# Kernel tuning notes

Measured on AMD Instinct MI355X. Metric: run time of the kernel, lower is better.

## Reference

```python
import jax, jax.numpy as jnp
import numpy as np
import math

NEG_INF = -1e9  # large negative used as masked-logit value (pre-scaling, as in the original)


def setup_inputs() -> dict:
    key = jax.random.key(0)
    k1, k2, k3 = jax.random.split(key, 3)
    bs, ql, kl, d = 8, 2048, 2048, 512
    return {
        "query": jax.random.normal(k1, (bs, ql, d), dtype=jnp.float32),
        "key": jax.random.normal(k2, (bs, kl, d), dtype=jnp.float32),
        "value": jax.random.normal(k3, (bs, kl, d), dtype=jnp.float32),
        "use_mask": 1,
        "cell_dim": 512,
    }


def reference(query, key, value, use_mask, cell_dim):
    bs, ql, d = query.shape[0], query.shape[1], value.shape[2]
    kl = key.shape[1]
    # [bs, ql, kl] raw scores
    mm = jnp.einsum("bqd,bkd->bqk", query, key)
    if use_mask:
        # mask positions where key index > query index (strictly future)
        q_idx = jnp.arange(ql)[:, None]
        k_idx = jnp.arange(kl)[None, :]
        mask = (k_idx > q_idx).astype(mm.dtype)  # [ql, kl]
        mm = mm + mask[None, :, :] * NEG_INF
    # log_softmax(...).exp() == softmax, computed stably in one pass
    w = jax.nn.softmax(mm / math.sqrt(cell_dim), axis=2)
    # weighted value aggregation (original broadcasts to [bs,ql,kl,d]; einsum fuses it)
    res = jnp.einsum("bqk,bkd->bqd", w, value)
    return res
```

## Files before the change

kernel.cpp:

```cpp
#include <hip/hip_runtime.h>
#include <math.h>

typedef __bf16 bf16x8 __attribute__((ext_vector_type(8)));
typedef float floatx4 __attribute__((ext_vector_type(4)));
typedef unsigned short ushort8_t __attribute__((ext_vector_type(8)));

#define BSZ 8
#define SEQ 2048
#define DIM 512
#define BKEY 32
#define BQ 128
#define NSLOT 70

__device__ __forceinline__ unsigned short f2bf(float f) {
    unsigned int u = __float_as_uint(f);
    u += 0x7fffu + ((u >> 16) & 1u);
    return (unsigned short)(u >> 16);
}
__device__ __forceinline__ float bf2f(unsigned short s) {
    return __uint_as_float(((unsigned int)s) << 16);
}

#define ASYNC16(g, l) __builtin_amdgcn_global_load_lds( \
    (const __attribute__((address_space(1))) unsigned int*)(g), \
    (__attribute__((address_space(3))) unsigned int*)(l), 16, 0, 0)

__global__ __launch_bounds__(256) void conv_k(const float* __restrict__ K,
                                              unsigned short* __restrict__ Kb) {
    size_t i = ((size_t)blockIdx.x * 256 + threadIdx.x) * 8;
    float4 a = *(const float4*)(K + i);
    float4 b = *(const float4*)(K + i + 4);
    ushort8_t u;
    u[0]=f2bf(a.x); u[1]=f2bf(a.y); u[2]=f2bf(a.z); u[3]=f2bf(a.w);
    u[4]=f2bf(b.x); u[5]=f2bf(b.y); u[6]=f2bf(b.z); u[7]=f2bf(b.w);
    *(ushort8_t*)(Kb + i) = u;
}

__global__ __launch_bounds__(256) void trans_v(const float* __restrict__ V,
                                               unsigned short* __restrict__ Vt) {
    __shared__ unsigned short T[BKEY][DIM + 8];
    const int bid = blockIdx.x;
    const int b = bid & 7, kb = bid >> 3;
    const float* src = V + ((size_t)b * SEQ + (size_t)kb * BKEY) * DIM;
    const int tid = threadIdx.x;
    #pragma unroll
    for (int i = 0; i < 16; ++i) {
        const int idx = i * 256 + tid;
        const int key = idx >> 7;
        const int d = (idx & 127) * 4;
        float4 x = *(const float4*)(src + (size_t)key * DIM + d);
        T[key][d]   = f2bf(x.x);
        T[key][d+1] = f2bf(x.y);
        T[key][d+2] = f2bf(x.z);
        T[key][d+3] = f2bf(x.w);
    }
    __syncthreads();
    unsigned short* dst = Vt + (size_t)(b * (SEQ / BKEY) + kb) * DIM * BKEY;
    #pragma unroll
    for (int i = 0; i < 8; ++i) {
        const int cidx = i * 256 + tid;
        const int d = cidx >> 2;
        const int kc = cidx & 3;
        ushort8_t v;
        #pragma unroll
        for (int k2 = 0; k2 < 8; ++k2) v[k2] = T[kc * 8 + k2][d];
        *(ushort8_t*)(dst + cidx * 8) = v;
    }
}


template <int SPLIT>
__global__ __launch_bounds__(512, 2)
void attn_fwd(const float* __restrict__ Q,
              const unsigned short* __restrict__ Kb,
              const unsigned short* __restrict__ Vt,
              unsigned short* __restrict__ PartO,
              float* __restrict__ Pml,
              float* __restrict__ O)
{
    __shared__ unsigned short Ksh[2][BKEY * DIM];
    __shared__ unsigned short Vsh[2][DIM * BKEY];
    __shared__ unsigned short Psh[8 * 16 * BKEY];

    const int tid  = threadIdx.x;
    const int lane = tid & 63;
    const int wv   = tid >> 6;
    const int ml   = lane & 15;
    const int quad = lane >> 4;

    const int bid = blockIdx.x;
    const int b   = bid & 7;
    const int j   = bid >> 3;
    int t, c;
    if (SPLIT) {
        t = 15; c = j;
        while (true) { const int cnt = (t + 2) >> 1; if (c < cnt) break; c -= cnt; --t; }
    } else { t = 15 - j; c = 0; }
    const int kt0 = c * 8;
    const int nk  = 4 * t + 4;
    const int kt1 = min(kt0 + 8, nk);
    const bool is_split = SPLIT && (t >= 2);
    const int q0 = t * BQ;
    const int kdiag = 4 * t;

    const float* Qb = Q + (size_t)b * SEQ * DIM;
    const unsigned short* Kbb = Kb + (size_t)b * SEQ * DIM;
    const unsigned short* Vtb = Vt + (size_t)b * SEQ * DIM;
    float* Ob = O + (size_t)b * SEQ * DIM;

    bf16x8 qf[16];
    {
        const float* qp = Qb + (size_t)(q0 + wv * 16 + ml) * DIM + quad * 8;
        #pragma unroll
        for (int kc = 0; kc < 16; ++kc) {
            float4 x = *(const float4*)(qp + kc * 32);
            float4 y = *(const float4*)(qp + kc * 32 + 4);
            union { bf16x8 v; unsigned short s[8]; } u;
            u.s[0]=f2bf(x.x); u.s[1]=f2bf(x.y); u.s[2]=f2bf(x.z); u.s[3]=f2bf(x.w);
            u.s[4]=f2bf(y.x); u.s[5]=f2bf(y.y); u.s[6]=f2bf(y.z); u.s[7]=f2bf(y.w);
            qf[kc] = u.v;
        }
    }
    asm volatile("" ::: "memory");

    floatx4 acc[32];
    #pragma unroll
    for (int i = 0; i < 32; ++i) acc[i] = (floatx4){0.f, 0.f, 0.f, 0.f};
    float mrun[4] = {-INFINITY, -INFINITY, -INFINITY, -INFINITY};
    float lrun[4] = {0.f, 0.f, 0.f, 0.f};

    const float CS = 1.4426950408889634f * 0.04419417382415922f;

    #define STAGE_K(buf_, kt_) do { \
        const unsigned short* Kt_ = Kbb + (size_t)(kt_) * (BKEY * DIM); \
        unsigned short* Kd_ = &Ksh[(buf_)][0]; \
        _Pragma("unroll") \
        for (int i_ = 0; i_ < 4; ++i_) { \
            const int ci_  = i_ * 512 + tid; \
            const int row_ = ci_ >> 6; \
            const int ch_  = (ci_ & 63) ^ (row_ & 7); \
            ASYNC16(Kt_ + (size_t)row_ * DIM + ch_ * 8, Kd_ + ci_ * 8); \
        } } while (0)
    #define STAGE_V(buf_, kt_) do { \
        const unsigned short* Vt_ = Vtb + (size_t)(kt_) * (DIM * BKEY); \
        unsigned short* Vd_ = &Vsh[(buf_)][0]; \
        _Pragma("unroll") \
        for (int i_ = 0; i_ < 4; ++i_) { \
            const int ci_ = i_ * 512 + tid; \
            const int d_  = ci_ >> 2; \
            const int kc_ = (ci_ & 3) ^ (d_ & 3); \
            ASYNC16(Vt_ + d_ * BKEY + kc_ * 8, Vd_ + ci_ * 8); \
        } } while (0)

    STAGE_K(0, kt0);
    STAGE_V(0, kt0);
    asm volatile("s_waitcnt vmcnt(4)" ::: "memory");
    __builtin_amdgcn_s_barrier();

    int cur = 0;
    for (int kt = kt0; kt < kt1; ++kt) {
        const int k0 = kt * BKEY;
        const bool havenxt = (kt + 1 < kt1);

        if (havenxt) STAGE_K(cur ^ 1, kt + 1);

        const unsigned short* Ks = &Ksh[cur][0];
        floatx4 s0 = (floatx4){0,0,0,0}, s1 = (floatx4){0,0,0,0};
        floatx4 s0b = (floatx4){0,0,0,0}, s1b = (floatx4){0,0,0,0};
        const int sw = ml & 7;
        __builtin_amdgcn_s_setprio(1);
        #pragma unroll
        for (int kc = 0; kc < 16; kc += 2) {
            const int ch0 = kc * 4 + quad, ch1 = (kc + 1) * 4 + quad;
            bf16x8 a0 = *(bf16x8*)&Ks[ml * DIM + ((ch0 ^ sw) << 3)];
            bf16x8 a1 = *(bf16x8*)&Ks[(16 + ml) * DIM + ((ch0 ^ sw) << 3)];
            bf16x8 b0 = *(bf16x8*)&Ks[ml * DIM + ((ch1 ^ sw) << 3)];
            bf16x8 b1 = *(bf16x8*)&Ks[(16 + ml) * DIM + ((ch1 ^ sw) << 3)];
            s0  = __builtin_amdgcn_mfma_f32_16x16x32_bf16(qf[kc],     a0, s0,  0, 0, 0);
            s1  = __builtin_amdgcn_mfma_f32_16x16x32_bf16(qf[kc],     a1, s1,  0, 0, 0);
            s0b = __builtin_amdgcn_mfma_f32_16x16x32_bf16(qf[kc + 1], b0, s0b, 0, 0, 0);
            s1b = __builtin_amdgcn_mfma_f32_16x16x32_bf16(qf[kc + 1], b1, s1b, 0, 0, 0);
        }
        __builtin_amdgcn_s_setprio(0);
        s0 = s0 + s0b;
        s1 = s1 + s1b;

        float z[2][4], pr[2][4], al[4], rs[4];
        if (kt >= kdiag) {
            #pragma unroll
            for (int r = 0; r < 4; ++r) {
                const int qg = q0 + wv * 16 + quad * 4 + r;
                z[0][r] = (k0 + ml > qg)      ? -INFINITY : s0[r] * CS;
                z[1][r] = (k0 + 16 + ml > qg) ? -INFINITY : s1[r] * CS;
            }
        } else {
            #pragma unroll
            for (int r = 0; r < 4; ++r) { z[0][r] = s0[r] * CS; z[1][r] = s1[r] * CS; }
        }
        #pragma unroll
        for (int r = 0; r < 4; ++r) {
            float v = fmaxf(z[0][r], z[1][r]);
            v = fmaxf(v, __shfl_xor(v, 1, 64));
            v = fmaxf(v, __shfl_xor(v, 2, 64));
            v = fmaxf(v, __shfl_xor(v, 4, 64));
            v = fmaxf(v, __shfl_xor(v, 8, 64));
            const float nm = fmaxf(mrun[r], v);
            al[r]   = __builtin_amdgcn_exp2f(mrun[r] - nm);
            mrun[r] = nm;
        }
        #pragma unroll
        for (int r = 0; r < 4; ++r) {
            pr[0][r] = __builtin_amdgcn_exp2f(z[0][r] - mrun[r]);
            pr[1][r] = __builtin_amdgcn_exp2f(z[1][r] - mrun[r]);
            float s = pr[0][r] + pr[1][r];
            s += __shfl_xor(s, 1, 64);
            s += __shfl_xor(s, 2, 64);
            s += __shfl_xor(s, 4, 64);
            s += __shfl_xor(s, 8, 64);
            rs[r] = s;
        }
        #pragma unroll
        for (int r = 0; r < 4; ++r) lrun[r] = lrun[r] * al[r] + rs[r];

        if (al[0] < 1.f || al[1] < 1.f || al[2] < 1.f || al[3] < 1.f) {
            #pragma unroll
            for (int nt = 0; nt < 32; ++nt) {
                acc[nt][0] *= al[0]; acc[nt][1] *= al[1];
                acc[nt][2] *= al[2]; acc[nt][3] *= al[3];
            }
        }

        unsigned short* Pw = &Psh[wv * (16 * BKEY)];
        #pragma unroll
        for (int nt = 0; nt < 2; ++nt) {
            #pragma unroll
            for (int r = 0; r < 4; ++r) {
                const int row = quad * 4 + r, col = nt * 16 + ml;
                Pw[row * BKEY + ((((col >> 3) ^ (row & 3)) << 3) | (col & 7))] = f2bf(pr[nt][r]);
            }
        }
        asm volatile("s_waitcnt lgkmcnt(0)" ::: "memory");
        bf16x8 pf = *(bf16x8*)&Pw[ml * BKEY + ((quad ^ (ml & 3)) << 3)];

        if (havenxt) { asm volatile("s_waitcnt vmcnt(4)" ::: "memory"); }
        else         { asm volatile("s_waitcnt vmcnt(0)" ::: "memory"); }
        __builtin_amdgcn_s_barrier();

        if (havenxt) STAGE_V(cur ^ 1, kt + 1);

        const unsigned short* Vs = &Vsh[cur][0];
        __builtin_amdgcn_s_setprio(1);
        #pragma unroll
        for (int nt = 0; nt < 32; ++nt) {
            const int drow = nt * 16 + ml;
            bf16x8 vf = *(bf16x8*)&Vs[drow * BKEY + ((quad ^ (drow & 3)) << 3)];
            acc[nt] = __builtin_amdgcn_mfma_f32_16x16x32_bf16(pf, vf, acc[nt], 0, 0, 0);
        }
        __builtin_amdgcn_s_setprio(0);

        if (havenxt) {
            asm volatile("s_waitcnt vmcnt(4)" ::: "memory");
            __builtin_amdgcn_s_barrier();
            cur ^= 1;
        }
    }
    #undef STAGE_K
    #undef STAGE_V

    if (!is_split) {
        float inv[4];
        #pragma unroll
        for (int r = 0; r < 4; ++r) inv[r] = 1.f / lrun[r];
        #pragma unroll
        for (int nt = 0; nt < 32; ++nt) {
            #pragma unroll
            for (int r = 0; r < 4; ++r) {
                const int row = q0 + wv * 16 + quad * 4 + r;
                Ob[(size_t)row * DIM + nt * 16 + ml] = acc[nt][r] * inv[r];
            }
        }
    } else {
        const size_t slot = (size_t)(b * NSLOT + j);
        unsigned short* po = PartO + slot * (BQ * DIM);
        #pragma unroll
        for (int nt = 0; nt < 32; ++nt) {
            #pragma unroll
            for (int r = 0; r < 4; ++r) {
                const int prow = wv * 16 + quad * 4 + r;
                po[prow * DIM + nt * 16 + ml] = f2bf(acc[nt][r]);
            }
        }
        if (ml == 0) {
            #pragma unroll
            for (int r = 0; r < 4; ++r) {
                const int prow = wv * 16 + quad * 4 + r;
                Pml[slot * 256 + prow * 2]     = mrun[r];
                Pml[slot * 256 + prow * 2 + 1] = lrun[r];
            }
        }
    }
}

__global__ __launch_bounds__(256)
void attn_merge(const unsigned short* __restrict__ PartO,
                const float* __restrict__ Pml,
                float* __restrict__ O)
{
    const int bid = blockIdx.x;
    const int b = bid & 7;
    const int u = bid >> 3;
    const int t = 2 + (u >> 2);
    const int rg = u & 3;
    const int nc = (t + 2) >> 1;
    int j0 = 0;
    for (int tp = 15; tp > t; --tp) j0 += (tp + 2) >> 1;

    const int r   = threadIdx.x >> 3;
    const int row = rg * 32 + r;
    const int d0  = (threadIdx.x & 7) * 64;

    float M = -INFINITY;
    for (int cc = 0; cc < nc; ++cc) {
        const size_t slot = (size_t)(b * NSLOT + j0 + cc);
        M = fmaxf(M, Pml[slot * 256 + row * 2]);
    }
    float L = 0.f;
    for (int cc = 0; cc < nc; ++cc) {
        const size_t slot = (size_t)(b * NSLOT + j0 + cc);
        L += Pml[slot * 256 + row * 2 + 1] *
             __builtin_amdgcn_exp2f(Pml[slot * 256 + row * 2] - M);
    }

    float o[64];
    #pragma unroll
    for (int i = 0; i < 64; ++i) o[i] = 0.f;
    for (int cc = 0; cc < nc; ++cc) {
        const size_t slot = (size_t)(b * NSLOT + j0 + cc);
        const float w = __builtin_amdgcn_exp2f(Pml[slot * 256 + row * 2] - M);
        const unsigned short* po = PartO + slot * (BQ * DIM) + (size_t)row * DIM + d0;
        #pragma unroll
        for (int i = 0; i < 8; ++i) {
            ushort8_t v = *(const ushort8_t*)(po + i * 8);
            #pragma unroll
            for (int k2 = 0; k2 < 8; ++k2) o[i * 8 + k2] += w * bf2f(v[k2]);
        }
    }
    const float invL = 1.f / L;
    float* out = O + ((size_t)b * SEQ + (size_t)t * BQ + row) * DIM + d0;
    #pragma unroll
    for (int i = 0; i < 16; ++i) {
        float4 v4 = { o[i*4] * invL, o[i*4+1] * invL, o[i*4+2] * invL, o[i*4+3] * invL };
        *(float4*)(out + i * 4) = v4;
    }
}

extern "C" void kernel_launch(void* const* d_in, const int* in_sizes, int n_in,
                              void* d_out, int out_size, void* d_ws, size_t ws_size,
                              hipStream_t stream) {
    const float* Q = (const float*)d_in[0];
    const float* K = (const float*)d_in[1];
    const float* V = (const float*)d_in[2];
    float* Out = (float*)d_out;

    const size_t elems = (size_t)BSZ * SEQ * DIM;
    unsigned short* Kb = (unsigned short*)d_ws;
    unsigned short* Vt = Kb + elems;
    unsigned short* PartO = Vt + elems;
    float* Pml = (float*)(PartO + (size_t)BSZ * NSLOT * BQ * DIM);

    const size_t need_split = 2 * elems * 2
                            + (size_t)BSZ * NSLOT * BQ * DIM * 2
                            + (size_t)BSZ * NSLOT * 256 * 4;
    conv_k<<<dim3(elems / 8 / 256), dim3(256), 0, stream>>>(K, Kb);
    trans_v<<<dim3(BSZ * (SEQ / BKEY)), dim3(256), 0, stream>>>(V, Vt);

    if (ws_size >= need_split) {
        attn_fwd<1><<<dim3(BSZ * 72), dim3(512), 0, stream>>>(Q, Kb, Vt, PartO, Pml, Out);
        attn_merge<<<dim3(BSZ * 14 * 4), dim3(256), 0, stream>>>(PartO, Pml, Out);
    } else {
        attn_fwd<0><<<dim3(BSZ * 16), dim3(512), 0, stream>>>(Q, Kb, Vt, PartO, Pml, Out);
    }
}
```

Before: 338.5 us.

## Shrink split-K chunks, fuse K/V prep kernels, and add lazy softmax rescaling

Parameterises the split-KV attention by chunk size and uses 6-key-tile chunks (96 blocks per batch) so work is spread more evenly across compute units, with a merge kernel that now covers more query tiles. The K conversion and V transpose kernels are merged into one launch to save a kernel launch. The online softmax now only raises the running max when the new max exceeds it by more than 8 in log2 units, which skips most accumulator rescales. The score registers are also reused in place for the probabilities. The lazy threshold allows exponentials up to 2^8 in bf16 P and fp32 sums, which is safe but changes rounding. Smaller chunks add partial-output traffic and merge work.

```diff
diff --git a/kernel.cpp b/kernel.cpp
--- a/kernel.cpp
+++ b/kernel.cpp
@@ -10,7 +10,6 @@
 #define DIM 512
 #define BKEY 32
 #define BQ 128
-#define NSLOT 70
 
 __device__ __forceinline__ unsigned short f2bf(float f) {
     unsigned int u = __float_as_uint(f);
@@ -25,21 +24,22 @@
     (const __attribute__((address_space(1))) unsigned int*)(g), \
     (__attribute__((address_space(3))) unsigned int*)(l), 16, 0, 0)
 
-__global__ __launch_bounds__(256) void conv_k(const float* __restrict__ K,
-                                              unsigned short* __restrict__ Kb) {
-    size_t i = ((size_t)blockIdx.x * 256 + threadIdx.x) * 8;
-    float4 a = *(const float4*)(K + i);
-    float4 b = *(const float4*)(K + i + 4);
-    ushort8_t u;
-    u[0]=f2bf(a.x); u[1]=f2bf(a.y); u[2]=f2bf(a.z); u[3]=f2bf(a.w);
-    u[4]=f2bf(b.x); u[5]=f2bf(b.y); u[6]=f2bf(b.z); u[7]=f2bf(b.w);
-    *(ushort8_t*)(Kb + i) = u;
-}
-
-__global__ __launch_bounds__(256) void trans_v(const float* __restrict__ V,
+__global__ __launch_bounds__(256) void prep_kv(const float* __restrict__ K,
+                                               const float* __restrict__ V,
+                                               unsigned short* __restrict__ Kb,
                                                unsigned short* __restrict__ Vt) {
+    if (blockIdx.x < 4096) {
+        size_t i = ((size_t)blockIdx.x * 256 + threadIdx.x) * 8;
+        float4 a = *(const float4*)(K + i);
+        float4 b = *(const float4*)(K + i + 4);
+        ushort8_t u;
+        u[0]=f2bf(a.x); u[1]=f2bf(a.y); u[2]=f2bf(a.z); u[3]=f2bf(a.w);
+        u[4]=f2bf(b.x); u[5]=f2bf(b.y); u[6]=f2bf(b.z); u[7]=f2bf(b.w);
+        *(ushort8_t*)(Kb + i) = u;
+        return;
+    }
     __shared__ unsigned short T[BKEY][DIM + 8];
-    const int bid = blockIdx.x;
+    const int bid = blockIdx.x - 4096;
     const int b = bid & 7, kb = bid >> 3;
     const float* src = V + ((size_t)b * SEQ + (size_t)kb * BKEY) * DIM;
     const int tid = threadIdx.x;
@@ -69,7 +69,7 @@
 }
 
 
-template <int SPLIT>
+template <int SPLIT, int CH, int NSLOT>
 __global__ __launch_bounds__(512, 2)
 void attn_fwd(const float* __restrict__ Q,
               const unsigned short* __restrict__ Kb,
@@ -94,12 +94,12 @@
     int t, c;
     if (SPLIT) {
         t = 15; c = j;
-        while (true) { const int cnt = (t + 2) >> 1; if (c < cnt) break; c -= cnt; --t; }
+        while (true) { const int cnt = (4 * t + 4 + CH - 1) / CH; if (c < cnt) break; c -= cnt; --t; }
     } else { t = 15 - j; c = 0; }
-    const int kt0 = c * 8;
     const int nk  = 4 * t + 4;
-    const int kt1 = min(kt0 + 8, nk);
-    const bool is_split = SPLIT && (t >= 2);
+    const int kt0 = c * CH;
+    const int kt1 = SPLIT ? min(kt0 + CH, nk) : nk;
+    const bool is_split = SPLIT && (nk > CH);
     const int q0 = t * BQ;
     const int kdiag = 4 * t;
 
@@ -126,7 +126,7 @@
     floatx4 acc[32];
     #pragma unroll
     for (int i = 0; i < 32; ++i) acc[i] = (floatx4){0.f, 0.f, 0.f, 0.f};
-    float mrun[4] = {-INFINITY, -INFINITY, -INFINITY, -INFINITY};
+    float mrun[4] = {-1e30f, -1e30f, -1e30f, -1e30f};
     float lrun[4] = {0.f, 0.f, 0.f, 0.f};
 
     const float CS = 1.4426950408889634f * 0.04419417382415922f;
@@ -185,42 +185,42 @@
         s0 = s0 + s0b;
         s1 = s1 + s1b;
 
-        float z[2][4], pr[2][4], al[4], rs[4];
         if (kt >= kdiag) {
             #pragma unroll
             for (int r = 0; r < 4; ++r) {
                 const int qg = q0 + wv * 16 + quad * 4 + r;
-                z[0][r] = (k0 + ml > qg)      ? -INFINITY : s0[r] * CS;
-                z[1][r] = (k0 + 16 + ml > qg) ? -INFINITY : s1[r] * CS;
+                s0[r] = (k0 + ml > qg)      ? -INFINITY : s0[r] * CS;
+                s1[r] = (k0 + 16 + ml > qg) ? -INFINITY : s1[r] * CS;
             }
         } else {
             #pragma unroll
-            for (int r = 0; r < 4; ++r) { z[0][r] = s0[r] * CS; z[1][r] = s1[r] * CS; }
-        }
+            for (int r = 0; r < 4; ++r) { s0[r] *= CS; s1[r] *= CS; }
+        }
+
+        float al[4];
         #pragma unroll
         for (int r = 0; r < 4; ++r) {
-            float v = fmaxf(z[0][r], z[1][r]);
+            float v = fmaxf(s0[r], s1[r]);
             v = fmaxf(v, __shfl_xor(v, 1, 64));
             v = fmaxf(v, __shfl_xor(v, 2, 64));
             v = fmaxf(v, __shfl_xor(v, 4, 64));
             v = fmaxf(v, __shfl_xor(v, 8, 64));
-            const float nm = fmaxf(mrun[r], v);
-            al[r]   = __builtin_amdgcn_exp2f(mrun[r] - nm);
-            mrun[r] = nm;
+            const float d = v - mrun[r];
+            const bool up = d > 8.0f;
+            al[r]   = up ? __builtin_amdgcn_exp2f(-d) : 1.0f;
+            mrun[r] = up ? v : mrun[r];
         }
         #pragma unroll
         for (int r = 0; r < 4; ++r) {
-            pr[0][r] = __builtin_amdgcn_exp2f(z[0][r] - mrun[r]);
-            pr[1][r] = __builtin_amdgcn_exp2f(z[1][r] - mrun[r]);
-            float s = pr[0][r] + pr[1][r];
-            s += __shfl_xor(s, 1, 64);
-            s += __shfl_xor(s, 2, 64);
-            s += __shfl_xor(s, 4, 64);
-            s += __shfl_xor(s, 8, 64);
-            rs[r] = s;
-        }
-        #pragma unroll
-        for (int r = 0; r < 4; ++r) lrun[r] = lrun[r] * al[r] + rs[r];
+            s0[r] = __builtin_amdgcn_exp2f(s0[r] - mrun[r]);
+            s1[r] = __builtin_amdgcn_exp2f(s1[r] - mrun[r]);
+            float rs = s0[r] + s1[r];
+            rs += __shfl_xor(rs, 1, 64);
+            rs += __shfl_xor(rs, 2, 64);
+            rs += __shfl_xor(rs, 4, 64);
+            rs += __shfl_xor(rs, 8, 64);
+            lrun[r] = lrun[r] * al[r] + rs;
+        }
 
         if (al[0] < 1.f || al[1] < 1.f || al[2] < 1.f || al[3] < 1.f) {
             #pragma unroll
@@ -232,12 +232,12 @@
 
         unsigned short* Pw = &Psh[wv * (16 * BKEY)];
         #pragma unroll
-        for (int nt = 0; nt < 2; ++nt) {
-            #pragma unroll
-            for (int r = 0; r < 4; ++r) {
-                const int row = quad * 4 + r, col = nt * 16 + ml;
-                Pw[row * BKEY + ((((col >> 3) ^ (row & 3)) << 3) | (col & 7))] = f2bf(pr[nt][r]);
-            }
+        for (int r = 0; r < 4; ++r) {
+            const int row = quad * 4 + r;
+            const int col0 = ml;
+            const int col1 = 16 + ml;
+            Pw[row * BKEY + ((((col0 >> 3) ^ (row & 3)) << 3) | (col0 & 7))] = f2bf(s0[r]);
+            Pw[row * BKEY + ((((col1 >> 3) ^ (row & 3)) << 3) | (col1 & 7))] = f2bf(s1[r]);
         }
         asm volatile("s_waitcnt lgkmcnt(0)" ::: "memory");
         bf16x8 pf = *(bf16x8*)&Pw[ml * BKEY + ((quad ^ (ml & 3)) << 3)];
@@ -301,6 +301,7 @@
     }
 }
 
+template <int CH, int NSLOT, int TMIN>
 __global__ __launch_bounds__(256)
 void attn_merge(const unsigned short* __restrict__ PartO,
                 const float* __restrict__ Pml,
@@ -309,14 +310,13 @@
     const int bid = blockIdx.x;
     const int b = bid & 7;
     const int u = bid >> 3;
-    const int t = 2 + (u >> 2);
+    const int t = TMIN + (u >> 2);
     const int rg = u & 3;
-    const int nc = (t + 2) >> 1;
+    const int nc = (4 * t + 4 + CH - 1) / CH;
     int j0 = 0;
-    for (int tp = 15; tp > t; --tp) j0 += (tp + 2) >> 1;
-
-    const int r   = threadIdx.x >> 3;
-    const int row = rg * 32 + r;
+    for (int tp = 15; tp > t; --tp) j0 += (4 * tp + 4 + CH - 1) / CH;
+
+    const int row = rg * 32 + (threadIdx.x >> 3);
     const int d0  = (threadIdx.x & 7) * 64;
 
     float M = -INFINITY;
@@ -366,18 +366,22 @@
     unsigned short* Kb = (unsigned short*)d_ws;
     unsigned short* Vt = Kb + elems;
     unsigned short* PartO = Vt + elems;
-    float* Pml = (float*)(PartO + (size_t)BSZ * NSLOT * BQ * DIM);
-
-    const size_t need_split = 2 * elems * 2
-                            + (size_t)BSZ * NSLOT * BQ * DIM * 2
-                            + (size_t)BSZ * NSLOT * 256 * 4;
-    conv_k<<<dim3(elems / 8 / 256), dim3(256), 0, stream>>>(K, Kb);
-    trans_v<<<dim3(BSZ * (SEQ / BKEY)), dim3(256), 0, stream>>>(V, Vt);
-
-    if (ws_size >= need_split) {
-        attn_fwd<1><<<dim3(BSZ * 72), dim3(512), 0, stream>>>(Q, Kb, Vt, PartO, Pml, Out);
-        attn_merge<<<dim3(BSZ * 14 * 4), dim3(256), 0, stream>>>(PartO, Pml, Out);
+    const size_t kvbytes = 2 * elems * 2;
+
+    prep_kv<<<dim3(4096 + BSZ * (SEQ / BKEY)), dim3(256), 0, stream>>>(K, V, Kb, Vt);
+
+    const size_t need6 = kvbytes + (size_t)BSZ * 95 * BQ * DIM * 2 + (size_t)BSZ * 95 * 256 * 4;
+    const size_t need8 = kvbytes + (size_t)BSZ * 70 * BQ * DIM * 2 + (size_t)BSZ * 70 * 256 * 4;
+
+    if (ws_size >= need6) {
+        float* Pml = (float*)(PartO + (size_t)BSZ * 95 * BQ * DIM);
+        attn_fwd<1, 6, 95><<<dim3(BSZ * 96), dim3(512), 0, stream>>>(Q, Kb, Vt, PartO, Pml, Out);
+        attn_merge<6, 95, 1><<<dim3(BSZ * 15 * 4), dim3(256), 0, stream>>>(PartO, Pml, Out);
+    } else if (ws_size >= need8) {
+        float* Pml = (float*)(PartO + (size_t)BSZ * 70 * BQ * DIM);
+        attn_fwd<1, 8, 70><<<dim3(BSZ * 72), dim3(512), 0, stream>>>(Q, Kb, Vt, PartO, Pml, Out);
+        attn_merge<8, 70, 2><<<dim3(BSZ * 14 * 4), dim3(256), 0, stream>>>(PartO, Pml, Out);
     } else {
-        attn_fwd<0><<<dim3(BSZ * 16), dim3(512), 0, stream>>>(Q, Kb, Vt, PartO, Pml, Out);
-    }
-}
+        attn_fwd<0, 8, 70><<<dim3(BSZ * 16), dim3(512), 0, stream>>>(Q, Kb, Vt, PartO, (float*)PartO, Out);
+    }
+}
```

After: 315.7 us. 1.07x faster.
